# Performance work log

Hardware: AMD Instinct MI355X
Metric: run time of the kernel (lower is better)

Reference implementation:

```python
import jax, jax.numpy as jnp
import numpy as np

N = 20000        # nodes
E = 160000       # edges
MUL = 64         # multiplicity per irrep (0e and 1o)
EDIM = 8         # scalar edge-embedding dim (radial basis)
NZ = 4           # node-attr (species one-hot) channels
AVG_NEIGH = 8.0  # avg_num_neighbors
INV_SQRT3 = float(1.0 / np.sqrt(3.0))  # CG norm for 1o x 1o -> 0e


def setup_inputs() -> dict:
    key = jax.random.key(0)
    ks = jax.random.split(key, 13)
    s = lambda fan: 1.0 / np.sqrt(fan)
    return {
        "node_feats": jax.random.normal(ks[0], (N, 256), jnp.float32),          # 64x0e | 64x1o (flattened)
        "node_attrs": jax.random.uniform(ks[1], (N, NZ), jnp.float32),
        "edge_attrs": jax.random.normal(ks[2], (E, 4), jnp.float32),            # SH lmax=1: [Y0 | Y1(3)]
        "edge_embedding": jax.random.normal(ks[3], (E, EDIM), jnp.float32),
        # linear_1 (per-irrep channel mixing)
        "W_lin1_0": jax.random.normal(ks[4], (MUL, MUL), jnp.float32),
        "W_lin1_1": jax.random.normal(ks[5], (MUL, MUL), jnp.float32),
        # radial MLP: EDIM -> EDIM -> 4*MUL tp weights
        "W_mlp1": jax.random.normal(ks[6], (EDIM, EDIM), jnp.float32),
        "W_mlp2": jax.random.normal(ks[7], (EDIM, 4 * MUL), jnp.float32),
        # linear_2: 128x0e+128x1o -> 128x0e+64x1o
        "W_lin2_0": jax.random.normal(ks[8], (2 * MUL, 2 * MUL), jnp.float32),
        "W_lin2_1": jax.random.normal(ks[9], (2 * MUL, MUL), jnp.float32),
        # self-connection FCTP weights: (u, z, w)
        "W_sc0": jax.random.normal(ks[10], (MUL, NZ, 2 * MUL), jnp.float32),
        "W_sc1": jax.random.normal(ks[11], (MUL, NZ, MUL), jnp.float32),
        "edge_index": jax.random.randint(ks[12], (2, E), 0, N, dtype=jnp.int32),
    }


def reference(node_feats, node_attrs, edge_attrs, edge_embedding,
              W_lin1_0, W_lin1_1, W_mlp1, W_mlp2,
              W_lin2_0, W_lin2_1, W_sc0, W_sc1, edge_index):
    edge_src, edge_dst = edge_index[0], edge_index[1]

    # split node feats into irrep blocks: 64x0e scalars, 64x1o vectors
    x0 = node_feats[:, :MUL]                         # [N, 64]
    x1 = node_feats[:, MUL:].reshape(N, MUL, 3)      # [N, 64, 3]

    # linear_1 (e3nn Linear, per-irrep, 1/sqrt(fan_in))
    inv = 1.0 / np.sqrt(MUL)
    h0 = (x0 @ W_lin1_0) * inv                       # [N, 64]
    h1 = jnp.einsum("nud,uv->nvd", x1, W_lin1_1) * inv

    # radial MLP -> per-edge UVU weights (e3nn FullyConnectedNet: no bias, silu, 1/sqrt(fan_in))
    inv_e = 1.0 / np.sqrt(EDIM)
    hid = jax.nn.silu((edge_embedding @ W_mlp1) * inv_e)
    w = (hid @ W_mlp2) * inv_e                       # [E, 4*MUL]
    w1, w2, w3, w4 = w[:, :MUL], w[:, MUL:2*MUL], w[:, 2*MUL:3*MUL], w[:, 3*MUL:]

    # gather source-node features per edge
    g0 = h0[edge_src]                                # [E, 64]
    g1 = h1[edge_src]                                # [E, 64, 3]
    a0 = edge_attrs[:, :1]                           # [E, 1]  Y0
    a1 = edge_attrs[:, 1:]                           # [E, 3]  Y1

    # UVU tensor product paths (v = 1 for SH attrs)
    m0_a = w1 * g0 * a0                              # 0e x 0e -> 0e
    m0_b = w4 * jnp.einsum("eud,ed->eu", g1, a1) * INV_SQRT3   # 1o x 1o -> 0e
    m1_a = (w2 * g0)[:, :, None] * a1[:, None, :]    # 0e x 1o -> 1o
    m1_b = (w3[:, :, None] * g1) * a0[:, :, None]    # 1o x 0e -> 1o
    msg0 = jnp.concatenate([m0_a, m0_b], axis=1)     # [E, 128]
    msg1 = jnp.concatenate([m1_a, m1_b], axis=1)     # [E, 128, 3]

    # scatter_add to destination nodes, normalize by sqrt(avg_num_neighbors)
    inv_n = 1.0 / np.sqrt(AVG_NEIGH)
    s0 = jax.ops.segment_sum(msg0, edge_dst, num_segments=N) * inv_n   # [N, 128]
    s1 = jax.ops.segment_sum(msg1, edge_dst, num_segments=N) * inv_n   # [N, 128, 3]

    # linear_2: 128x0e+128x1o -> 128x0e (64 scalars + 64 gates) + 64x1o
    inv2 = 1.0 / np.sqrt(2 * MUL)
    u0 = (s0 @ W_lin2_0) * inv2                      # [N, 128]
    u1 = jnp.einsum("nud,uw->nwd", s1, W_lin2_1) * inv2   # [N, 64, 3]

    # self-connection FCTP with 0e node attrs (species-conditioned linear)
    inv_sc = 1.0 / np.sqrt(MUL * NZ)
    sc0 = jnp.einsum("nu,nz,uzw->nw", x0, node_attrs, W_sc0) * inv_sc
    sc1 = jnp.einsum("nud,nz,uzw->nwd", x1, node_attrs, W_sc1) * inv_sc
    t0 = u0 + sc0                                    # [N, 128]
    t1 = u1 + sc1                                    # [N, 64, 3]

    # Gate nonlinearity: silu on scalars, silu(gates) * vectors
    scalars = jax.nn.silu(t0[:, :MUL])               # [N, 64]
    gates = jax.nn.silu(t0[:, MUL:])                 # [N, 64]
    vectors = gates[:, :, None] * t1                 # [N, 64, 3]

    out = jnp.concatenate([scalars, vectors.reshape(N, MUL * 3)], axis=1)  # [N, 256]
    # resnet (irreps match input)
    return node_feats + out
```

## Files before the change

kernel.cpp:

```cpp
#include <hip/hip_runtime.h>
#include <hip/hip_bf16.h>
#include <math.h>

#define N 20000
#define E 160000
#define MUL 64
#define EDIM 8
#define NZ 4

#define INV_SQRT_MUL 0.125f
#define INV_E 0.35355339059327373f
#define INV_N 0.35355339059327373f
#define INV2 0.08838834764831845f
#define INV_SC 0.0625f
#define INV_SQRT3 0.5773502691896258f

typedef unsigned short u16;
typedef unsigned int u32;
typedef short bf16x8 __attribute__((ext_vector_type(8)));
typedef float f32x4 __attribute__((ext_vector_type(4)));

__device__ __forceinline__ float silu(float v) {
    return v / (1.0f + __expf(-v));
}
__device__ __forceinline__ u16 f2bf(float f) {
    union { float f; unsigned int u; } v; v.f = f;
    unsigned int r = (v.u + 0x7FFFu + ((v.u >> 16) & 1u)) >> 16;
    return (u16)r;
}
__device__ __forceinline__ float bflo(u32 p) {
    union { unsigned int u; float f; } v; v.u = p << 16; return v.f;
}
__device__ __forceinline__ float bfhi(u32 p) {
    union { unsigned int u; float f; } v; v.u = p & 0xFFFF0000u; return v.f;
}
#define MFMA(a, b, c) __builtin_amdgcn_mfma_f32_16x16x32_bf16(a, b, c, 0, 0, 0)

__device__ __forceinline__ void gll16(const u16* g, u16* l) {
    __builtin_amdgcn_global_load_lds(
        (const __attribute__((address_space(1))) u32*)g,
        (__attribute__((address_space(3))) u32*)l, 16, 0, 0);
}


#define PREP_B  5000
#define WCONV_B 320
#define HID_B   5000
#define LIST_B  625

__global__ __launch_bounds__(256) void k_front(
    const float* __restrict__ x,
    const float* __restrict__ eemb, const int* __restrict__ eidx,
    const float* __restrict__ W20, const float* __restrict__ Wsc0,
    const float* __restrict__ W21, const float* __restrict__ Wsc1,
    const float* __restrict__ W0, const float* __restrict__ W1,
    const float* __restrict__ Wm1,
    u16* __restrict__ A1, u16* __restrict__ x1p,
    u16* __restrict__ Bt1m, u16* __restrict__ Bt1z, u16* __restrict__ Bt2,
    u16* __restrict__ W0b, u16* __restrict__ W1b,
    float* __restrict__ hid, int* __restrict__ head, int2* __restrict__ nl)
{
    const int b = blockIdx.x;
    const int tid = threadIdx.x;
    __shared__ float xr[4][256];

    if (b < PREP_B) {
        const int n0 = b * 4;
        #pragma unroll
        for (int t = 0; t < 4; ++t)
            xr[t][tid] = x[(size_t)(n0 + t) * 256 + tid];
        __syncthreads();
        #pragma unroll
        for (int t = 0; t < 4; ++t) {
            const int n = n0 + t;
            if (tid < 64) {
                A1[(size_t)n * 192 + 128 + tid] = f2bf(xr[t][tid]);
            } else {
                int q = tid - 64;
                int d = q >> 6, uu = q & 63;
                x1p[((size_t)n * 3 + d) * 64 + uu] = f2bf(xr[t][64 + uu * 3 + d]);
            }
        }
    } else if (b < PREP_B + WCONV_B) {
        int i = (b - PREP_B) * 256 + tid;
        if (i < 16384) {
            int w = i >> 7, k = i & 127;
            Bt1m[i] = f2bf(W20[k * 128 + w]);
        } else if (i < 49152) {
            int j = i - 16384;
            int z = j >> 13, r = j & 8191, w = r >> 6, k = r & 63;
            Bt1z[j] = f2bf(Wsc0[(k * 4 + z) * 128 + w] * INV_SC);
        } else if (i < 73728) {
            int j = i - 49152;
            int w = j / 384, k = j % 384;
            float v = (k < 128) ? W21[k * 64 + w] : Wsc1[(k - 128) * 64 + w];
            Bt2[j] = f2bf(v);
        } else if (i < 77824) {
            int j = i - 73728;
            int v = j >> 6, u = j & 63;
            W0b[j] = f2bf(W0[u * 64 + v] * INV_SQRT_MUL);
        } else {
            int j = i - 77824;
            int v = j >> 6, u = j & 63;
            W1b[j] = f2bf(W1[u * 64 + v] * INV_SQRT_MUL);
        }
    } else if (b < PREP_B + WCONV_B + HID_B) {
        int i = (b - PREP_B - WCONV_B) * 256 + tid;
        int e = i >> 3, k = i & 7;
        float s = 0.f;
        #pragma unroll
        for (int j = 0; j < 8; ++j)
            s += eemb[(size_t)e * 8 + j] * Wm1[j * 8 + k];
        hid[i] = silu(s * INV_E);
    } else {
        int e = (b - PREP_B - WCONV_B - HID_B) * 256 + tid;
        if (e < E) {
            int src = eidx[e];
            int dst = eidx[E + e];
            int old = atomicExch(&head[dst], e);
            nl[e] = make_int2(old, src);
        }
    }
}

__global__ __launch_bounds__(256) void k_hgemm(
    const u16* __restrict__ A1, const u16* __restrict__ x1p,
    const u16* __restrict__ W0b, const u16* __restrict__ W1b,
    u16* __restrict__ hc)
{
    const int lane = threadIdx.x & 63;
    const int g = blockIdx.x * 4 + (threadIdx.x >> 6);
    const int quad = lane >> 4, l16 = lane & 15;
    const bool isC1 = (g >= 1250);
    const int row0 = isC1 ? (g - 1250) * 16 : g * 16;
    const u16* Ap = isC1 ? (x1p + (size_t)(row0 + l16) * 64)
                         : (A1 + (size_t)(row0 + l16) * 192 + 128);
    const u16* Bp = isC1 ? W1b : W0b;

    f32x4 acc[4] = {};
    #pragma unroll
    for (int k0 = 0; k0 < 64; k0 += 32) {
        bf16x8 a = *(const bf16x8*)(Ap + k0 + quad * 8);
        #pragma unroll
        for (int ct = 0; ct < 4; ++ct) {
            bf16x8 bb = *(const bf16x8*)(Bp + (size_t)(ct * 16 + l16) * 64 + k0 + quad * 8);
            acc[ct] = MFMA(a, bb, acc[ct]);
        }
    }
    #pragma unroll
    for (int ct = 0; ct < 4; ++ct) {
        #pragma unroll
        for (int r = 0; r < 4; ++r) {
            int row = row0 + quad * 4 + r;
            int vv = ct * 16 + l16;
            if (!isC1) {
                hc[(size_t)row * 256 + vv * 4] = f2bf(acc[ct][r]);
            } else {
                int n = row / 3, d = row - 3 * (row / 3);
                hc[(size_t)n * 256 + vv * 4 + 1 + d] = f2bf(acc[ct][r]);
            }
        }
    }
}

__global__ __launch_bounds__(256) void k_gather(
    const int* __restrict__ head, const int2* __restrict__ nl,
    const float* __restrict__ eattr, const float* __restrict__ hid,
    const u32* __restrict__ hc2, const float* __restrict__ Wm2,
    u16* __restrict__ A1, u16* __restrict__ A2g)
{
    const int lane = threadIdx.x & 63;
    const int n = blockIdx.x * 4 + (threadIdx.x >> 6);

    float wm0[8], wm1[8], wm2r[8], wm3[8];
    #pragma unroll
    for (int k = 0; k < 8; ++k) {
        wm0[k]  = Wm2[k * 256 + lane];
        wm1[k]  = Wm2[k * 256 + 64 + lane];
        wm2r[k] = Wm2[k * 256 + 128 + lane];
        wm3[k]  = Wm2[k * 256 + 192 + lane];
    }

    float acc0a = 0.f, acc0b = 0.f;
    float s1a[3] = {0.f, 0.f, 0.f}, s1b[3] = {0.f, 0.f, 0.f};

    int e0 = head[n];
    if (e0 != -1) {
        int2 v0 = nl[e0];
        float4 ea = ((const float4*)eattr)[e0];
        float4 hA = ((const float4*)hid)[(size_t)e0 * 2];
        float4 hB = ((const float4*)hid)[(size_t)e0 * 2 + 1];
        uint2  hp = ((const uint2*)hc2)[(size_t)v0.y * 64 + lane];
        int e1 = v0.x;
        int2 v1 = make_int2(-1, 0);
        if (e1 != -1) v1 = nl[e1];

        while (true) {
            int e2 = -1;
            int2 v2 = make_int2(-1, 0);
            float4 eaN, hAN, hBN; uint2 hpN;
            if (e1 != -1) {
                e2 = v1.x;
                if (e2 != -1) v2 = nl[e2];
                eaN = ((const float4*)eattr)[e1];
                hAN = ((const float4*)hid)[(size_t)e1 * 2];
                hBN = ((const float4*)hid)[(size_t)e1 * 2 + 1];
                hpN = ((const uint2*)hc2)[(size_t)v1.y * 64 + lane];
            }

            float w1 = hA.x*wm0[0]+hA.y*wm0[1]+hA.z*wm0[2]+hA.w*wm0[3]
                     + hB.x*wm0[4]+hB.y*wm0[5]+hB.z*wm0[6]+hB.w*wm0[7];
            float w2 = hA.x*wm1[0]+hA.y*wm1[1]+hA.z*wm1[2]+hA.w*wm1[3]
                     + hB.x*wm1[4]+hB.y*wm1[5]+hB.z*wm1[6]+hB.w*wm1[7];
            float w3 = hA.x*wm2r[0]+hA.y*wm2r[1]+hA.z*wm2r[2]+hA.w*wm2r[3]
                     + hB.x*wm2r[4]+hB.y*wm2r[5]+hB.z*wm2r[6]+hB.w*wm2r[7];
            float w4 = hA.x*wm3[0]+hA.y*wm3[1]+hA.z*wm3[2]+hA.w*wm3[3]
                     + hB.x*wm3[4]+hB.y*wm3[5]+hB.z*wm3[6]+hB.w*wm3[7];
            const float g0 = bflo(hp.x), g1x = bfhi(hp.x);
            const float g1y = bflo(hp.y), g1z = bfhi(hp.y);
            acc0a += w1 * g0 * ea.x;
            acc0b += w4 * (g1x * ea.y + g1y * ea.z + g1z * ea.w);
            const float wg = w2 * g0, w3a = w3 * ea.x;
            s1a[0] += wg * ea.y;  s1a[1] += wg * ea.z;  s1a[2] += wg * ea.w;
            s1b[0] += w3a * g1x;  s1b[1] += w3a * g1y;  s1b[2] += w3a * g1z;

            if (e1 == -1) break;
            ea = eaN; hA = hAN; hB = hBN; hp = hpN;
            e1 = e2; v1 = v2;
        }
    }

    const float f = INV_E * INV_N * INV2;
    u16* a1p = &A1[(size_t)n * 192];
    a1p[lane]      = f2bf(acc0a * f);
    a1p[64 + lane] = f2bf(acc0b * f * INV_SQRT3);
    #pragma unroll
    for (int d = 0; d < 3; ++d) {
        u16* a2p = &A2g[((size_t)n * 3 + d) * 128];
        a2p[lane]      = f2bf(s1a[d] * f);
        a2p[64 + lane] = f2bf(s1b[d] * f);
    }
}

__global__ __launch_bounds__(512, 4) void k_gemm_fused(
    const u16* __restrict__ A1, const u16* __restrict__ A2g,
    const u16* __restrict__ x1p,
    const u16* __restrict__ Bt1m, const u16* __restrict__ Bt1z,
    const u16* __restrict__ Bt2,
    const float* __restrict__ attrs, const float* __restrict__ x,
    float* __restrict__ out)
{
    const int lane = threadIdx.x & 63;
    const int wave = threadIdx.x >> 6;
    const int quad = lane >> 4, l16 = lane & 15;
    const int n0 = blockIdx.x * 16;
    const float4* at4 = (const float4*)attrs;

    __shared__ __align__(16) u16 sA1[16 * 192];
    __shared__ __align__(16) u16 sA2[48 * 128];
    __shared__ float st0[16][132];
    __shared__ float st1[48][68];

    {
        const u16* gA1 = A1 + (size_t)n0 * 192;
        const u16* gA2 = A2g + (size_t)(3 * n0) * 128;
        #pragma unroll
        for (int i = 0; i < 3; ++i) {
            const int cc = wave + i * 8;
            if (cc < 6) {
                const int Lu = cc * 512 + lane * 8;
                const int row = Lu / 192;
                const int src = Lu ^ ((row & 7) << 3);
                gll16(gA1 + src, &sA1[cc * 512]);
            } else if (cc < 18) {
                const int Lu = (cc - 6) * 512 + lane * 8;
                const int row = Lu >> 7;
                const int src = Lu ^ ((row & 7) << 3);
                gll16(gA2 + src, &sA2[(cc - 6) * 512]);
            }
        }
    }

    const u16 *bz0p = nullptr, *bz1p = nullptr;
    bf16x8 PB[8], PC[8];
    u32 XQ[3][8];
    float4 atv[3];

    if (wave < 4) {
        const u16* b0p = Bt1m + (size_t)(wave * 16 + l16) * 128 + quad * 8;
        const u16* b1p = Bt1m + (size_t)((wave + 4) * 16 + l16) * 128 + quad * 8;
        bz0p = Bt1z + (size_t)(wave * 16 + l16) * 64 + quad * 8;
        bz1p = Bt1z + (size_t)((wave + 4) * 16 + l16) * 64 + quad * 8;
        #pragma unroll
        for (int kt = 0; kt < 4; ++kt) {
            PB[kt]     = *(const bf16x8*)(b0p + kt * 32);
            PB[4 + kt] = *(const bf16x8*)(b1p + kt * 32);
        }
        #pragma unroll
        for (int z = 0; z < 2; ++z)
            #pragma unroll
            for (int kt = 0; kt < 2; ++kt) {
                PC[z * 2 + kt]     = *(const bf16x8*)(bz0p + z * 8192 + kt * 32);
                PC[4 + z * 2 + kt] = *(const bf16x8*)(bz1p + z * 8192 + kt * 32);
            }
    } else {
        const int ct = wave - 4;
        const u16* b2p = Bt2 + (size_t)(ct * 16 + l16) * 384 + quad * 8;
        const u16* xq0 = x1p + (size_t)(3 * n0 + l16) * 64 + quad * 2;
        #pragma unroll
        for (int kt = 0; kt < 4; ++kt)
            PB[kt] = *(const bf16x8*)(b2p + kt * 32);
        #pragma unroll
        for (int kt = 0; kt < 8; ++kt) {
            bf16x8 v = *(const bf16x8*)(b2p + 128 + kt * 32);
            if (kt < 4) PB[4 + kt] = v; else PC[kt - 4] = v;
        }
        #pragma unroll
        for (int rt = 0; rt < 3; ++rt)
            #pragma unroll
            for (int kt = 0; kt < 8; ++kt)
                XQ[rt][kt] = *(const u32*)(xq0 + rt * 16 * 64 + kt * 8);
        #pragma unroll
        for (int rt = 0; rt < 3; ++rt) {
            const int ro = rt * 16 + l16;
            const int nn = (ro * 21846) >> 16;
            const float4 v = at4[n0 + nn];
            atv[rt].x = v.x * INV_SC; atv[rt].y = v.y * INV_SC;
            atv[rt].z = v.z * INV_SC; atv[rt].w = v.w * INV_SC;
        }
    }

    const int c = threadIdx.x & 255;
    const int th = threadIdx.x >> 8;
    float xv[8];
    #pragma unroll
    for (int i = 0; i < 8; ++i)
        xv[i] = x[(size_t)(n0 + i * 2 + th) * 256 + c];

    __syncthreads();

    if (wave < 4) {
        f32x4 m0 = {}, m1 = {};
        #pragma unroll
        for (int kt = 0; kt < 4; ++kt) {
            const int off = l16 * 192 + kt * 32 + quad * 8;
            bf16x8 a0 = *(const bf16x8*)(sA1 + (off ^ ((l16 & 7) << 3)));
            m0 = MFMA(a0, PB[kt], m0);
            m1 = MFMA(a0, PB[4 + kt], m1);
        }
        bf16x8 a0s[2];
        #pragma unroll
        for (int kt = 0; kt < 2; ++kt) {
            const int off = l16 * 192 + 128 + kt * 32 + quad * 8;
            a0s[kt] = *(const bf16x8*)(sA1 + (off ^ ((l16 & 7) << 3)));
        }
        f32x4 z0[4] = {}, z1[4] = {};
        #pragma unroll
        for (int z = 0; z < 2; ++z)
            #pragma unroll
            for (int kt = 0; kt < 2; ++kt) {
                z0[z] = MFMA(a0s[kt], PC[z * 2 + kt], z0[z]);
                z1[z] = MFMA(a0s[kt], PC[4 + z * 2 + kt], z1[z]);
            }
        #pragma unroll
        for (int z = 0; z < 2; ++z)
            #pragma unroll
            for (int kt = 0; kt < 2; ++kt) {
                bf16x8 d0 = *(const bf16x8*)(bz0p + (z + 2) * 8192 + kt * 32);
                bf16x8 d1 = *(const bf16x8*)(bz1p + (z + 2) * 8192 + kt * 32);
                z0[z + 2] = MFMA(a0s[kt], d0, z0[z + 2]);
                z1[z + 2] = MFMA(a0s[kt], d1, z1[z + 2]);
            }

        #pragma unroll
        for (int r = 0; r < 4; ++r) {
            const int r0 = quad * 4 + r;
            const float4 a = at4[n0 + r0];
            st0[r0][wave * 16 + l16] =
                m0[r] + a.x * z0[0][r] + a.y * z0[1][r] + a.z * z0[2][r] + a.w * z0[3][r];
            st0[r0][(wave + 4) * 16 + l16] =
                m1[r] + a.x * z1[0][r] + a.y * z1[1][r] + a.z * z1[2][r] + a.w * z1[3][r];
        }
    } else {
        const int ct = wave - 4;
        f32x4 mt[3] = {};
        #pragma unroll
        for (int kt = 0; kt < 4; ++kt) {
            #pragma unroll
            for (int rt = 0; rt < 3; ++rt) {
                const int row = rt * 16 + l16;
                const int off = row * 128 + kt * 32 + quad * 8;
                bf16x8 a = *(const bf16x8*)(sA2 + (off ^ ((row & 7) << 3)));
                mt[rt] = MFMA(a, PB[kt], mt[rt]);
            }
        }
        #pragma unroll
        for (int kt = 0; kt < 8; ++kt) {
            const bf16x8 b2 = (kt < 4) ? PB[4 + kt] : PC[kt - 4];
            #pragma unroll
            for (int rt = 0; rt < 3; ++rt) {
                const u32 xp = XQ[rt][kt];
                const float xa = bflo(xp), xb = bfhi(xp);
                bf16x8 af;
                af[0] = (short)f2bf(xa * atv[rt].x); af[1] = (short)f2bf(xa * atv[rt].y);
                af[2] = (short)f2bf(xa * atv[rt].z); af[3] = (short)f2bf(xa * atv[rt].w);
                af[4] = (short)f2bf(xb * atv[rt].x); af[5] = (short)f2bf(xb * atv[rt].y);
                af[6] = (short)f2bf(xb * atv[rt].z); af[7] = (short)f2bf(xb * atv[rt].w);
                mt[rt] = MFMA(af, b2, mt[rt]);
            }
        }

        #pragma unroll
        for (int r = 0; r < 4; ++r) {
            const int r0 = quad * 4 + r;
            st1[r0][ct * 16 + l16]      = mt[0][r];
            st1[16 + r0][ct * 16 + l16] = mt[1][r];
            st1[32 + r0][ct * 16 + l16] = mt[2][r];
        }
    }

    __syncthreads();

    #pragma unroll
    for (int i = 0; i < 8; ++i) {
        const int t = i * 2 + th;
        float o;
        if (c < 64) {
            o = xv[i] + silu(st0[t][c]);
        } else {
            int r = c - 64;
            int w = (r * 21846) >> 16;
            int d = r - w * 3;
            o = xv[i] + silu(st0[t][64 + w]) * st1[t * 3 + d][w];
        }
        out[(size_t)(n0 + t) * 256 + c] = o;
    }
}

extern "C" void kernel_launch(void* const* d_in, const int* in_sizes, int n_in,
                              void* d_out, int out_size, void* d_ws, size_t ws_size,
                              hipStream_t stream) {
    const float* node_feats = (const float*)d_in[0];
    const float* node_attrs = (const float*)d_in[1];
    const float* edge_attrs = (const float*)d_in[2];
    const float* edge_emb   = (const float*)d_in[3];
    const float* W_lin1_0   = (const float*)d_in[4];
    const float* W_lin1_1   = (const float*)d_in[5];
    const float* W_mlp1     = (const float*)d_in[6];
    const float* W_mlp2     = (const float*)d_in[7];
    const float* W_lin2_0   = (const float*)d_in[8];
    const float* W_lin2_1   = (const float*)d_in[9];
    const float* W_sc0      = (const float*)d_in[10];
    const float* W_sc1      = (const float*)d_in[11];
    const int*   edge_index = (const int*)d_in[12];
    float* out = (float*)d_out;

    char* p = (char*)d_ws;
    float* hid = (float*)p;                 p += (size_t)E * 8 * 4;
    u16* hc    = (u16*)p;                   p += (size_t)N * 256 * 2;
    u16* A1    = (u16*)p;                   p += (size_t)N * 192 * 2;
    u16* A2g   = (u16*)p;                   p += (size_t)N * 3 * 128 * 2;
    u16* x1p   = (u16*)p;                   p += (size_t)N * 3 * 64 * 2;
    u16* Bt1m  = (u16*)p;                   p += 16384 * 2;
    u16* Bt1z  = (u16*)p;                   p += 32768 * 2;
    u16* Bt2   = (u16*)p;                   p += 24576 * 2;
    u16* W0b   = (u16*)p;                   p += 4096 * 2;
    u16* W1b   = (u16*)p;                   p += 4096 * 2;
    int* head  = (int*)p;                   p += N * 4;
    int2* nl   = (int2*)p;                  p += (size_t)E * 8;

    hipMemsetAsync(head, 0xFF, N * sizeof(int), stream);

    k_front<<<PREP_B + WCONV_B + HID_B + LIST_B, 256, 0, stream>>>(
        node_feats, edge_emb, edge_index,
        W_lin2_0, W_sc0, W_lin2_1, W_sc1, W_lin1_0, W_lin1_1, W_mlp1,
        A1, x1p, Bt1m, Bt1z, Bt2, W0b, W1b, hid, head, nl);
    k_hgemm<<<1250, 256, 0, stream>>>(A1, x1p, W0b, W1b, hc);
    k_gather<<<N / 4, 256, 0, stream>>>(head, nl, edge_attrs, hid,
                                        (const u32*)hc, W_mlp2, A1, A2g);
    k_gemm_fused<<<1250, 512, 0, stream>>>(A1, A2g, x1p, Bt1m, Bt1z, Bt2,
                                           node_attrs, node_feats, out);
}
```

Baseline: 205.4 us.

## Fuse linear_1 MFMA GEMM into front prep kernel via LDS-staged tiles

```diff
diff --git a/kernel.cpp b/kernel.cpp
--- a/kernel.cpp
+++ b/kernel.cpp
@@ -43,8 +43,8 @@
 }
 
 
-#define PREP_B  5000
-#define WCONV_B 320
+#define PREP_B  1250
+#define WCONV_B 288
 #define HID_B   5000
 #define LIST_B  625
 
@@ -57,32 +57,96 @@
     const float* __restrict__ Wm1,
     u16* __restrict__ A1, u16* __restrict__ x1p,
     u16* __restrict__ Bt1m, u16* __restrict__ Bt1z, u16* __restrict__ Bt2,
-    u16* __restrict__ W0b, u16* __restrict__ W1b,
-    float* __restrict__ hid, int* __restrict__ head, int2* __restrict__ nl)
+    u16* __restrict__ hc, float* __restrict__ hid,
+    int* __restrict__ head, int2* __restrict__ nl)
 {
     const int b = blockIdx.x;
     const int tid = threadIdx.x;
-    __shared__ float xr[4][256];
 
     if (b < PREP_B) {
-        const int n0 = b * 4;
-        #pragma unroll
-        for (int t = 0; t < 4; ++t)
+        __shared__ float xr[16][256];
+        __shared__ u16 sxb0[16 * 68];
+        __shared__ u16 sxb1[48 * 68];
+        const int n0 = b * 16;
+        const int lane = tid & 63, wave = tid >> 6;
+        const int quad = lane >> 4, l16 = lane & 15;
+
+        const float* Wsrc = (wave == 0) ? W0 : W1;
+        bf16x8 bw[4][2];
+        #pragma unroll
+        for (int ct = 0; ct < 4; ++ct)
+            #pragma unroll
+            for (int kk = 0; kk < 2; ++kk)
+                #pragma unroll
+                for (int j = 0; j < 8; ++j)
+                    bw[ct][kk][j] = (short)f2bf(
+                        Wsrc[(kk * 32 + quad * 8 + j) * 64 + ct * 16 + l16]
+                        * INV_SQRT_MUL);
+
+        #pragma unroll
+        for (int t = 0; t < 16; ++t)
             xr[t][tid] = x[(size_t)(n0 + t) * 256 + tid];
         __syncthreads();
-        #pragma unroll
-        for (int t = 0; t < 4; ++t) {
-            const int n = n0 + t;
-            if (tid < 64) {
-                A1[(size_t)n * 192 + 128 + tid] = f2bf(xr[t][tid]);
-            } else {
-                int q = tid - 64;
-                int d = q >> 6, uu = q & 63;
-                x1p[((size_t)n * 3 + d) * 64 + uu] = f2bf(xr[t][64 + uu * 3 + d]);
-            }
+
+        #pragma unroll
+        for (int i = 0; i < 4; ++i) {
+            const int idx = tid * 4 + i;
+            const int row = idx >> 6, col = idx & 63;
+            const u16 v = f2bf(xr[row][col]);
+            sxb0[row * 68 + col] = v;
+            A1[(size_t)(n0 + row) * 192 + 128 + col] = v;
+        }
+        #pragma unroll
+        for (int i = 0; i < 12; ++i) {
+            const int idx = tid * 12 + i;
+            const int lrow = idx >> 6, u = idx & 63;
+            const int t = (lrow * 21846) >> 16;
+            const int d = lrow - t * 3;
+            const u16 v = f2bf(xr[t][64 + u * 3 + d]);
+            sxb1[lrow * 68 + u] = v;
+            x1p[((size_t)(3 * n0) + lrow) * 64 + u] = v;
+        }
+        __syncthreads();
+
+        f32x4 acc[4] = {};
+        if (wave == 0) {
+            #pragma unroll
+            for (int kk = 0; kk < 2; ++kk) {
+                bf16x8 a = *(const bf16x8*)(sxb0 + l16 * 68 + kk * 32 + quad * 8);
+                #pragma unroll
+                for (int ct = 0; ct < 4; ++ct)
+                    acc[ct] = MFMA(a, bw[ct][kk], acc[ct]);
+            }
+            #pragma unroll
+            for (int ct = 0; ct < 4; ++ct)
+                #pragma unroll
+                for (int r = 0; r < 4; ++r) {
+                    const int row = n0 + quad * 4 + r;
+                    const int vv = ct * 16 + l16;
+                    hc[(size_t)row * 256 + vv * 4] = f2bf(acc[ct][r]);
+                }
+        } else {
+            const int rt = wave - 1;
+            #pragma unroll
+            for (int kk = 0; kk < 2; ++kk) {
+                bf16x8 a = *(const bf16x8*)(sxb1 + (rt * 16 + l16) * 68 + kk * 32 + quad * 8);
+                #pragma unroll
+                for (int ct = 0; ct < 4; ++ct)
+                    acc[ct] = MFMA(a, bw[ct][kk], acc[ct]);
+            }
+            #pragma unroll
+            for (int ct = 0; ct < 4; ++ct)
+                #pragma unroll
+                for (int r = 0; r < 4; ++r) {
+                    const int lrow = rt * 16 + quad * 4 + r;
+                    const int t = (lrow * 21846) >> 16;
+                    const int d = lrow - t * 3;
+                    const int vv = ct * 16 + l16;
+                    hc[(size_t)(n0 + t) * 256 + vv * 4 + 1 + d] = f2bf(acc[ct][r]);
+                }
         }
     } else if (b < PREP_B + WCONV_B) {
-        int i = (b - PREP_B) * 256 + tid;
+        const int i = (b - PREP_B) * 256 + tid;
         if (i < 16384) {
             int w = i >> 7, k = i & 127;
             Bt1m[i] = f2bf(W20[k * 128 + w]);
@@ -90,75 +154,27 @@
             int j = i - 16384;
             int z = j >> 13, r = j & 8191, w = r >> 6, k = r & 63;
             Bt1z[j] = f2bf(Wsc0[(k * 4 + z) * 128 + w] * INV_SC);
-        } else if (i < 73728) {
+        } else {
             int j = i - 49152;
             int w = j / 384, k = j % 384;
             float v = (k < 128) ? W21[k * 64 + w] : Wsc1[(k - 128) * 64 + w];
             Bt2[j] = f2bf(v);
-        } else if (i < 77824) {
-            int j = i - 73728;
-            int v = j >> 6, u = j & 63;
-            W0b[j] = f2bf(W0[u * 64 + v] * INV_SQRT_MUL);
-        } else {
-            int j = i - 77824;
-            int v = j >> 6, u = j & 63;
-            W1b[j] = f2bf(W1[u * 64 + v] * INV_SQRT_MUL);
         }
     } else if (b < PREP_B + WCONV_B + HID_B) {
-        int i = (b - PREP_B - WCONV_B) * 256 + tid;
-        int e = i >> 3, k = i & 7;
+        const int i = (b - PREP_B - WCONV_B) * 256 + tid;
+        const int e = i >> 3, k = i & 7;
         float s = 0.f;
         #pragma unroll
         for (int j = 0; j < 8; ++j)
             s += eemb[(size_t)e * 8 + j] * Wm1[j * 8 + k];
         hid[i] = silu(s * INV_E);
     } else {
-        int e = (b - PREP_B - WCONV_B - HID_B) * 256 + tid;
+        const int e = (b - PREP_B - WCONV_B - HID_B) * 256 + tid;
         if (e < E) {
             int src = eidx[e];
             int dst = eidx[E + e];
             int old = atomicExch(&head[dst], e);
             nl[e] = make_int2(old, src);
-        }
-    }
-}
-
-__global__ __launch_bounds__(256) void k_hgemm(
-    const u16* __restrict__ A1, const u16* __restrict__ x1p,
-    const u16* __restrict__ W0b, const u16* __restrict__ W1b,
-    u16* __restrict__ hc)
-{
-    const int lane = threadIdx.x & 63;
-    const int g = blockIdx.x * 4 + (threadIdx.x >> 6);
-    const int quad = lane >> 4, l16 = lane & 15;
-    const bool isC1 = (g >= 1250);
-    const int row0 = isC1 ? (g - 1250) * 16 : g * 16;
-    const u16* Ap = isC1 ? (x1p + (size_t)(row0 + l16) * 64)
-                         : (A1 + (size_t)(row0 + l16) * 192 + 128);
-    const u16* Bp = isC1 ? W1b : W0b;
-
-    f32x4 acc[4] = {};
-    #pragma unroll
-    for (int k0 = 0; k0 < 64; k0 += 32) {
-        bf16x8 a = *(const bf16x8*)(Ap + k0 + quad * 8);
-        #pragma unroll
-        for (int ct = 0; ct < 4; ++ct) {
-            bf16x8 bb = *(const bf16x8*)(Bp + (size_t)(ct * 16 + l16) * 64 + k0 + quad * 8);
-            acc[ct] = MFMA(a, bb, acc[ct]);
-        }
-    }
-    #pragma unroll
-    for (int ct = 0; ct < 4; ++ct) {
-        #pragma unroll
-        for (int r = 0; r < 4; ++r) {
-            int row = row0 + quad * 4 + r;
-            int vv = ct * 16 + l16;
-            if (!isC1) {
-                hc[(size_t)row * 256 + vv * 4] = f2bf(acc[ct][r]);
-            } else {
-                int n = row / 3, d = row - 3 * (row / 3);
-                hc[(size_t)n * 256 + vv * 4 + 1 + d] = f2bf(acc[ct][r]);
-            }
         }
     }
 }
@@ -464,8 +480,6 @@
     u16* Bt1m  = (u16*)p;                   p += 16384 * 2;
     u16* Bt1z  = (u16*)p;                   p += 32768 * 2;
     u16* Bt2   = (u16*)p;                   p += 24576 * 2;
-    u16* W0b   = (u16*)p;                   p += 4096 * 2;
-    u16* W1b   = (u16*)p;                   p += 4096 * 2;
     int* head  = (int*)p;                   p += N * 4;
     int2* nl   = (int2*)p;                  p += (size_t)E * 8;
 
@@ -474,8 +488,7 @@
     k_front<<<PREP_B + WCONV_B + HID_B + LIST_B, 256, 0, stream>>>(
         node_feats, edge_emb, edge_index,
         W_lin2_0, W_sc0, W_lin2_1, W_sc1, W_lin1_0, W_lin1_1, W_mlp1,
-        A1, x1p, Bt1m, Bt1z, Bt2, W0b, W1b, hid, head, nl);
-    k_hgemm<<<1250, 256, 0, stream>>>(A1, x1p, W0b, W1b, hc);
+        A1, x1p, Bt1m, Bt1z, Bt2, hc, hid, head, nl);
     k_gather<<<N / 4, 256, 0, stream>>>(head, nl, edge_attrs, hid,
                                         (const u32*)hc, W_mlp2, A1, A2g);
     k_gemm_fused<<<1250, 512, 0, stream>>>(A1, A2g, x1p, Bt1m, Bt1z, Bt2,
```

Measured after the change: 201.5 us. About the same (-1.9%).
